# Kernel optimization log

Measured on AMD Instinct MI355X. Metric: run time of the kernel, lower is better.

## Reference

```python
import jax, jax.numpy as jnp
import numpy as np


def setup_inputs() -> dict:
    key = jax.random.key(0)
    ks = jax.random.split(key, 16)
    B, T, A, R, M, D = 128, 1024, 512, 1024, 256, 256  # batch, max_time, annot, rnn, memory, attn dims
    F, K = 32, 31  # location filters, kernel size
    s = jnp.float32(0.02)
    return dict(
        memory=jax.random.normal(ks[0], (B, M), jnp.float32),
        context=jax.random.normal(ks[1], (B, A), jnp.float32),
        rnn_state=jax.random.normal(ks[2], (B, R), jnp.float32),
        annots=jax.random.normal(ks[3], (B, T, A), jnp.float32),
        atten=jax.random.uniform(ks[4], (B, 2, T), jnp.float32),
        mask=jax.random.randint(ks[5], (B, T), 0, 2).astype(jnp.int32),
        Wi=jax.random.normal(ks[6], (3 * R, A + M), jnp.float32) * s,   # GRU input weights (r,z,n)
        Wh=jax.random.normal(ks[7], (3 * R, R), jnp.float32) * s,       # GRU hidden weights
        bi=jnp.zeros((3 * R,), jnp.float32),
        bh=jnp.zeros((3 * R,), jnp.float32),
        conv_w=jax.random.normal(ks[8], (F, 2, K), jnp.float32) * s,    # loc_conv (OIH)
        loc_w=jax.random.normal(ks[9], (D, F), jnp.float32) * s,
        loc_b=jnp.zeros((D,), jnp.float32),
        q_w=jax.random.normal(ks[10], (D, R), jnp.float32) * s,
        q_b=jnp.zeros((D,), jnp.float32),
        a_w=jax.random.normal(ks[11], (D, A), jnp.float32) * s,
        a_b=jnp.zeros((D,), jnp.float32),
        v_w=jax.random.normal(ks[12], (1, D), jnp.float32) * s,
    )


def reference(memory, context, rnn_state, annots, atten, mask,
              Wi, Wh, bi, bh, conv_w, loc_w, loc_b, q_w, q_b, a_w, a_b, v_w):
    # --- GRUCell (torch gate order: r, z, n) ---
    x = jnp.concatenate([memory, context], axis=-1)          # (B, M+A)
    gi = x @ Wi.T + bi                                        # (B, 3R)
    gh = rnn_state @ Wh.T + bh                                # (B, 3R)
    ir, iz, inn = jnp.split(gi, 3, axis=-1)
    hr, hz, hn = jnp.split(gh, 3, axis=-1)
    r = jax.nn.sigmoid(ir + hr)
    z = jax.nn.sigmoid(iz + hz)
    n = jnp.tanh(inn + r * hn)
    h = (1.0 - z) * n + z * rnn_state                         # (B, R) rnn_output

    # --- Location-sensitive attention ---
    pad = (conv_w.shape[-1] - 1) // 2
    loc = jax.lax.conv_general_dilated(atten, conv_w, (1,), [(pad, pad)],
                                       dimension_numbers=('NCH', 'OIH', 'NCH'))  # (B, F, T)
    ploc = jnp.einsum('bft,df->btd', loc, loc_w) + loc_b      # (B, T, D)
    pq = (h @ q_w.T + q_b)[:, None, :]                        # (B, 1, D)
    pa = jnp.einsum('bta,da->btd', annots, a_w) + a_b         # (B, T, D)
    align = jnp.einsum('btd,d->bt', jnp.tanh(pq + pa + ploc), v_w[0])  # (B, T)

    # masked softmax (mask==0 -> -inf)
    align = jnp.where(mask != 0, align, jnp.float32(-1e30))
    align = jax.nn.softmax(align, axis=-1)

    # context = bmm(align, annots)
    ctx = jnp.einsum('bt,bta->ba', align, annots)             # (B, A)
    return (h, ctx, align)
```

## Files before the change

### kernel.cpp

```cpp
#include <hip/hip_runtime.h>
#include <cstddef>

constexpr int B  = 128;
constexpr int T  = 1024;
constexpr int AD = 512;
constexpr int R  = 1024;
constexpr int M  = 256;
constexpr int DD = 256;
constexpr int F  = 32;
constexpr int KW = 31;
constexpr int PADW = 15;
constexpr int XDIM = M + AD;
constexpr int G3 = 3 * R;
constexpr size_t BG3 = (size_t)B * G3;

using short8 = __attribute__((ext_vector_type(8))) short;
using f32x4  = __attribute__((ext_vector_type(4))) float;

__device__ __forceinline__ float sigmoidf(float x) { return 1.f / (1.f + __expf(-x)); }

__device__ __forceinline__ unsigned short f2bf(float x) {
  unsigned int u = __float_as_uint(x);
  u += 0x7FFFu + ((u >> 16) & 1u);
  return (unsigned short)(u >> 16);
}

__device__ __forceinline__ float tanh_fast(float x) {
  float e = __expf(2.f * x);
  return 1.f - 2.f / (e + 1.f);
}

__device__ __forceinline__ uint4 pack_bf8(float4 f0, float4 f1) {
  uint4 r;
  r.x = f2bf(f0.x) | ((unsigned)f2bf(f0.y) << 16);
  r.y = f2bf(f0.z) | ((unsigned)f2bf(f0.w) << 16);
  r.z = f2bf(f1.x) | ((unsigned)f2bf(f1.y) << 16);
  r.w = f2bf(f1.z) | ((unsigned)f2bf(f1.w) << 16);
  return r;
}

__device__ __forceinline__ void load_lds16(const void* g, void* l) {
  __builtin_amdgcn_global_load_lds(
      (const __attribute__((address_space(1))) unsigned int*)g,
      (__attribute__((address_space(3))) unsigned int*)l, 16, 0, 0);
}

__global__ __launch_bounds__(256) void prep_wsw(const float* __restrict__ aw,
                                                const float* __restrict__ lw,
                                                unsigned short* __restrict__ awsw,
                                                unsigned short* __restrict__ lwsw) {
  int idx = blockIdx.x * 256 + threadIdx.x;
  int chunk = idx >> 10;
  int rn = (idx & 1023) >> 2;
  int u = idx & 3;
  int su = u ^ ((rn >> 1) & 3);
  const float* src;
  unsigned short* dst;
  if (chunk < 16) {
    src = aw + (size_t)rn * AD + chunk * 32 + u * 8;
    dst = awsw + chunk * 8192 + rn * 32 + su * 8;
  } else {
    src = lw + (size_t)rn * F + u * 8;
    dst = lwsw + rn * 32 + su * 8;
  }
  float4 f0 = *(const float4*)src;
  float4 f1 = *(const float4*)(src + 4);
  *(uint4*)dst = pack_bf8(f0, f1);
}

__global__ __launch_bounds__(256) void prep_gru(const float* __restrict__ mem,
                                                const float* __restrict__ ctxin,
                                                const float* __restrict__ rnn,
                                                const float* __restrict__ Wi,
                                                const float* __restrict__ Wh,
                                                unsigned short* __restrict__ Wib,
                                                unsigned short* __restrict__ Whb,
                                                unsigned short* __restrict__ xb,
                                                unsigned short* __restrict__ rnnb) {
  const int t = blockIdx.x * 256 + threadIdx.x;
  const float* src;
  unsigned short* dst;
  if (t < 294912) {
    src = Wi + (size_t)t * 8;
    dst = Wib + (size_t)t * 8;
  } else if (t < 688128) {
    size_t e = (size_t)(t - 294912) * 8;
    src = Wh + e;
    dst = Whb + e;
  } else if (t < 700416) {
    size_t e = (size_t)(t - 688128) * 8;
    int row = (int)(e / XDIM), col = (int)(e % XDIM);
    src = (col < M) ? (mem + (size_t)row * M + col)
                    : (ctxin + (size_t)row * AD + (col - M));
    dst = xb + e;
  } else {
    size_t e = (size_t)(t - 700416) * 8;
    src = rnn + e;
    dst = rnnb + e;
  }
  float4 f0 = *(const float4*)src;
  float4 f1 = *(const float4*)(src + 4);
  *(uint4*)dst = pack_bf8(f0, f1);
}

__global__ __launch_bounds__(256) void loc_conv(const float* __restrict__ atten,
                                                const float* __restrict__ conv_w,
                                                unsigned short* __restrict__ locw) {
  __shared__ float s_att[2 * 94];
  __shared__ float s_cw[F * 62];
  const int tid = threadIdx.x;
  const int t0 = blockIdx.x * 64, b = blockIdx.y;
  for (int i = tid; i < 2 * 94; i += 256) {
    int c = i / 94, ii = i - c * 94;
    int gt = t0 - PADW + ii;
    s_att[i] = (gt >= 0 && gt < T) ? atten[((size_t)b * 2 + c) * T + gt] : 0.f;
  }
  for (int i = tid; i < F * 62; i += 256) s_cw[i] = conv_w[i];
  __syncthreads();
  const int f = tid & 31;
  const int tb = (tid >> 5) * 8;
  float a8[8] = {0.f, 0.f, 0.f, 0.f, 0.f, 0.f, 0.f, 0.f};
#pragma unroll
  for (int c = 0; c < 2; ++c) {
    float win[38];
#pragma unroll
    for (int i = 0; i < 38; ++i) win[i] = s_att[c * 94 + tb + i];
#pragma unroll
    for (int k = 0; k < KW; ++k) {
      float w = s_cw[f * 62 + c * 31 + k];
#pragma unroll
      for (int ti = 0; ti < 8; ++ti) a8[ti] += w * win[ti + k];
    }
  }
#pragma unroll
  for (int ti = 0; ti < 8; ++ti)
    locw[((size_t)b * T + t0 + tb + ti) * F + f] = f2bf(a8[ti]);
}

__global__ __launch_bounds__(256, 2) void gemm_gru(const unsigned short* __restrict__ xb,
                                                   const unsigned short* __restrict__ rnnb,
                                                   const unsigned short* __restrict__ Wib,
                                                   const unsigned short* __restrict__ Whb,
                                                   float* __restrict__ outp) {
  const int tid = threadIdx.x;
  const int wv = tid >> 6, lane = tid & 63;
  const int lm = lane & 15, lg = lane >> 4;
  const int g0 = blockIdx.x * 64;
  const int z = blockIdx.y;
  const int which = z >> 2, q = z & 3;
  const unsigned short* __restrict__ A = which ? rnnb : xb;
  const unsigned short* __restrict__ W = which ? Whb : Wib;
  const int K = which ? R : XDIM;
  const int Kq = K >> 2;
  const int nch = Kq >> 5;
  float* __restrict__ C = outp + (size_t)z * BG3;

  const unsigned short* aA = A + (size_t)(wv * 32 + lm) * K + q * Kq + lg * 8;
  const unsigned short* bW = W + (size_t)(g0 + lm) * K + q * Kq + lg * 8;

  f32x4 acc[2][4];
#pragma unroll
  for (int i = 0; i < 2; ++i)
#pragma unroll
    for (int j = 0; j < 4; ++j) acc[i][j] = (f32x4){0.f, 0.f, 0.f, 0.f};

#pragma unroll 2
  for (int ch = 0; ch < nch; ++ch) {
    const int k = ch * 32;
    short8 a8[2], b8[4];
#pragma unroll
    for (int i = 0; i < 2; ++i)
      a8[i] = *(const short8*)(aA + (size_t)i * 16 * K + k);
#pragma unroll
    for (int j = 0; j < 4; ++j)
      b8[j] = *(const short8*)(bW + (size_t)j * 16 * K + k);
#pragma unroll
    for (int j = 0; j < 4; ++j)
#pragma unroll
      for (int i = 0; i < 2; ++i)
        acc[i][j] = __builtin_amdgcn_mfma_f32_16x16x32_bf16(a8[i], b8[j], acc[i][j], 0, 0, 0);
  }

#pragma unroll
  for (int i = 0; i < 2; ++i)
#pragma unroll
    for (int reg = 0; reg < 4; ++reg) {
      const size_t row = (size_t)(wv * 32 + i * 16 + lg * 4 + reg) * G3 + g0 + lm;
#pragma unroll
      for (int j = 0; j < 4; ++j) C[row + j * 16] = acc[i][j][reg];
    }
}

__global__ __launch_bounds__(256) void gru_combine(const float* __restrict__ gp,
                                                   const float* __restrict__ bi,
                                                   const float* __restrict__ bh,
                                                   const float* __restrict__ hprev,
                                                   float* __restrict__ hout) {
  int idx = blockIdx.x * 256 + threadIdx.x;
  int b = idx >> 10, j = idx & (R - 1);
  float ir = bi[j], iz = bi[R + j], inn = bi[2 * R + j];
  float hr = bh[j], hz = bh[R + j], hn = bh[2 * R + j];
#pragma unroll
  for (int z = 0; z < 4; ++z) {
    const float* g = gp + (size_t)z * BG3 + (size_t)b * G3;
    ir += g[j]; iz += g[R + j]; inn += g[2 * R + j];
  }
#pragma unroll
  for (int z = 4; z < 8; ++z) {
    const float* g = gp + (size_t)z * BG3 + (size_t)b * G3;
    hr += g[j]; hz += g[R + j]; hn += g[2 * R + j];
  }
  float r = sigmoidf(ir + hr);
  float z = sigmoidf(iz + hz);
  float n = tanhf(inn + r * hn);
  float hp = hprev[(size_t)b * R + j];
  hout[(size_t)b * R + j] = (1.f - z) * n + z * hp;
}

__global__ __launch_bounds__(256) void pq_kernel(const float* __restrict__ h,
                                                 const float* __restrict__ q_w,
                                                 const float* __restrict__ q_b,
                                                 float* __restrict__ pq) {
  __shared__ __align__(16) float sh[R];
  int b = blockIdx.x, tid = threadIdx.x;
  ((float4*)sh)[tid] = ((const float4*)(h + (size_t)b * R))[tid];
  __syncthreads();
  const float* wr = q_w + (size_t)tid * R;
  float acc = 0.f;
#pragma unroll 4
  for (int k = 0; k < R; k += 4) {
    float4 w = *(const float4*)&wr[k];
    float4 x = *(const float4*)&sh[k];
    acc += w.x * x.x + w.y * x.y + w.z * x.z + w.w * x.w;
  }
  pq[(size_t)b * DD + tid] = acc + q_b[tid];
}

__global__ __launch_bounds__(256, 4) void attn_fused(
    const float* __restrict__ annots, const unsigned short* __restrict__ locw,
    const int* __restrict__ mask,
    const unsigned short* __restrict__ awsw, const unsigned short* __restrict__ lwsw,
    const float* __restrict__ loc_b, const float* __restrict__ a_b,
    const float* __restrict__ v_w, const float* __restrict__ pq,
    float* __restrict__ u_out, float* __restrict__ ctx_part,
    float* __restrict__ S_part) {
  __shared__ __align__(16) unsigned short s_A[2][64 * 32];
  __shared__ __align__(16) unsigned short s_B[2][256 * 32];

  const int tid = threadIdx.x;
  const int wv = tid >> 6, lane = tid & 63;
  const int lm = lane & 15, lg = lane >> 4;
  const int g = blockIdx.x, b = blockIdx.y;
  const int t0 = g * 64;
  const int ar = tid >> 2, au = tid & 3;
  const int asu = au ^ ((ar >> 1) & 3);
  const int sufb = lg ^ ((lm >> 1) & 3);

  const float* arow = annots + ((size_t)b * T + t0 + ar) * AD + au * 8;

  {
    float4 f0 = *(const float4*)(arow);
    float4 f1 = *(const float4*)(arow + 4);
#pragma unroll
    for (int kq = 0; kq < 4; ++kq)
      load_lds16(awsw + wv * 2048 + kq * 512 + lane * 8, &s_B[0][wv * 2048 + kq * 512]);
    *(uint4*)&s_A[0][ar * 32 + asu * 8] = pack_bf8(f0, f1);
  }
  float4 aN0 = *(const float4*)(arow + 32);
  float4 aN1 = *(const float4*)(arow + 36);
  uint4 lvN = {0, 0, 0, 0};

  f32x4 acc[4][4];
#pragma unroll
  for (int j = 0; j < 4; ++j) {
    int d = wv * 64 + j * 16 + lm;
    float base = pq[(size_t)b * DD + d] + a_b[d] + loc_b[d];
    f32x4 bv = {base, base, base, base};
#pragma unroll
    for (int i = 0; i < 4; ++i) acc[i][j] = bv;
  }
  asm volatile("s_waitcnt vmcnt(2) lgkmcnt(0)" ::: "memory");
  __builtin_amdgcn_s_barrier();

#pragma unroll 1
  for (int ks = 0; ks <= 16; ++ks) {
    const int cur = ks & 1, nxt = cur ^ 1;
    if (ks + 1 <= 16) {
      const unsigned short* img = (ks + 1 < 16) ? (awsw + (ks + 1) * 8192) : lwsw;
#pragma unroll
      for (int kq = 0; kq < 4; ++kq)
        load_lds16(img + wv * 2048 + kq * 512 + lane * 8,
                   &s_B[nxt][wv * 2048 + kq * 512]);
    }
    float4 aN20, aN21;
    uint4 lvN2;
    if (ks + 2 <= 15) {
      aN20 = *(const float4*)(arow + (ks + 2) * 32);
      aN21 = *(const float4*)(arow + (ks + 2) * 32 + 4);
    } else if (ks + 2 == 16) {
      lvN2 = *(const uint4*)(locw + ((size_t)b * T + t0 + ar) * F + au * 8);
    }
    if (ks + 1 <= 15) {
      *(uint4*)&s_A[nxt][ar * 32 + asu * 8] = pack_bf8(aN0, aN1);
    } else if (ks + 1 == 16) {
      *(uint4*)&s_A[nxt][ar * 32 + asu * 8] = lvN;
    }
    short8 afr[4], bfr[4];
#pragma unroll
    for (int i = 0; i < 4; ++i)
      afr[i] = *(const short8*)&s_A[cur][(i * 16 + lm) * 32 + sufb * 8];
#pragma unroll
    for (int j = 0; j < 4; ++j)
      bfr[j] = *(const short8*)&s_B[cur][(wv * 64 + j * 16 + lm) * 32 + sufb * 8];
#pragma unroll
    for (int j = 0; j < 4; ++j)
#pragma unroll
      for (int i = 0; i < 4; ++i)
        acc[i][j] = __builtin_amdgcn_mfma_f32_16x16x32_bf16(afr[i], bfr[j], acc[i][j], 0, 0, 0);
    if (ks <= 13) {
      asm volatile("s_waitcnt vmcnt(2) lgkmcnt(0)" ::: "memory");
    } else if (ks == 14) {
      asm volatile("s_waitcnt vmcnt(1) lgkmcnt(0)" ::: "memory");
    } else {
      asm volatile("s_waitcnt vmcnt(0) lgkmcnt(0)" ::: "memory");
    }
    __builtin_amdgcn_s_barrier();
    if (ks + 2 <= 15) { aN0 = aN20; aN1 = aN21; }
    else if (ks + 2 == 16) lvN = lvN2;
  }

  float* s_e = (float*)s_A;
  float* s_u = s_e + 256;
  float vwv[4];
#pragma unroll
  for (int j = 0; j < 4; ++j) vwv[j] = v_w[wv * 64 + j * 16 + lm];
#pragma unroll
  for (int i = 0; i < 4; ++i) {
#pragma unroll
    for (int reg = 0; reg < 4; ++reg) {
      float p = 0.f;
#pragma unroll
      for (int j = 0; j < 4; ++j) p += vwv[j] * tanh_fast(acc[i][j][reg]);
      p += __shfl_xor(p, 1);
      p += __shfl_xor(p, 2);
      p += __shfl_xor(p, 4);
      p += __shfl_xor(p, 8);
      if (lm == 0) s_e[wv * 64 + i * 16 + lg * 4 + reg] = p;
    }
  }
  __syncthreads();
  if (tid < 64) {
    float e = s_e[tid] + s_e[64 + tid] + s_e[128 + tid] + s_e[192 + tid];
    bool mk = mask[(size_t)b * T + t0 + tid] != 0;
    float u = mk ? __expf(e) : 0.f;
    u_out[(size_t)b * T + t0 + tid] = u;
    s_u[tid] = u;
    float p = u;
    p += __shfl_xor(p, 1);
    p += __shfl_xor(p, 2);
    p += __shfl_xor(p, 4);
    p += __shfl_xor(p, 8);
    p += __shfl_xor(p, 16);
    p += __shfl_xor(p, 32);
    if (tid == 0) S_part[b * 16 + g] = p;
  }
  __syncthreads();
  {
    const int a0 = tid * 2;
    const float* ap = annots + ((size_t)b * T + t0) * AD + a0;
    float c0 = 0.f, c1 = 0.f;
#pragma unroll 4
    for (int t = 0; t < 64; ++t) {
      float2 v = *(const float2*)(ap + (size_t)t * AD);
      float w = s_u[t];
      c0 += w * v.x;
      c1 += w * v.y;
    }
    float* dst = ctx_part + (size_t)g * ((size_t)B * AD) + (size_t)b * AD + a0;
    dst[0] = c0;
    dst[1] = c1;
  }
}

__global__ __launch_bounds__(512) void finalize(const float* __restrict__ S_part,
                                                const float* __restrict__ ctx_part,
                                                float* __restrict__ al,
                                                float* __restrict__ ctxo) {
  int b = blockIdx.x, tid = threadIdx.x;
  float S = 0.f;
#pragma unroll
  for (int g = 0; g < 16; ++g) S += S_part[b * 16 + g];
  float inv = 1.f / S;
  float2* ap = (float2*)(al + (size_t)b * T);
  float2 v = ap[tid];
  v.x *= inv; v.y *= inv;
  ap[tid] = v;
  float c = 0.f;
#pragma unroll
  for (int p = 0; p < 16; ++p)
    c += ctx_part[(size_t)p * ((size_t)B * AD) + (size_t)b * AD + tid];
  ctxo[(size_t)b * AD + tid] = c * inv;
}

extern "C" void kernel_launch(void* const* d_in, const int* in_sizes, int n_in,
                              void* d_out, int out_size, void* d_ws, size_t ws_size,
                              hipStream_t stream) {
  const float* memory = (const float*)d_in[0];
  const float* context = (const float*)d_in[1];
  const float* rnn = (const float*)d_in[2];
  const float* annots = (const float*)d_in[3];
  const float* atten = (const float*)d_in[4];
  const int* mask = (const int*)d_in[5];
  const float* Wi = (const float*)d_in[6];
  const float* Wh = (const float*)d_in[7];
  const float* bi = (const float*)d_in[8];
  const float* bh = (const float*)d_in[9];
  const float* conv_w = (const float*)d_in[10];
  const float* loc_w = (const float*)d_in[11];
  const float* loc_b = (const float*)d_in[12];
  const float* q_w = (const float*)d_in[13];
  const float* q_b = (const float*)d_in[14];
  const float* a_w = (const float*)d_in[15];
  const float* a_b = (const float*)d_in[16];
  const float* v_w = (const float*)d_in[17];

  float* out = (float*)d_out;
  float* out_h = out;
  float* out_ctx = out + (size_t)B * R;
  float* out_al = out_ctx + (size_t)B * AD;

  float* ws = (float*)d_ws;
  float* gp_ws = ws;
  float* pq_ws = gp_ws + 8 * BG3;
  float* S_part = pq_ws + (size_t)B * DD;
  float* ctx_part = S_part + (size_t)B * 16;
  unsigned short* awsw = (unsigned short*)(ctx_part + (size_t)16 * B * AD);
  unsigned short* lwsw = awsw + (size_t)16 * 8192;
  unsigned short* locw = lwsw + 8192;
  unsigned short* Wib = locw + (size_t)B * T * F;
  unsigned short* Whb = Wib + (size_t)G3 * XDIM;
  unsigned short* xb = Whb + (size_t)G3 * R;
  unsigned short* rnnb = xb + (size_t)B * XDIM;

  prep_wsw<<<68, 256, 0, stream>>>(a_w, loc_w, awsw, lwsw);
  prep_gru<<<2800, 256, 0, stream>>>(memory, context, rnn, Wi, Wh,
                                     Wib, Whb, xb, rnnb);
  loc_conv<<<dim3(T / 64, B), 256, 0, stream>>>(atten, conv_w, locw);
  gemm_gru<<<dim3(48, 8), 256, 0, stream>>>(xb, rnnb, Wib, Whb, gp_ws);
  gru_combine<<<(B * R) / 256, 256, 0, stream>>>(gp_ws, bi, bh, rnn, out_h);
  pq_kernel<<<B, 256, 0, stream>>>(out_h, q_w, q_b, pq_ws);
  attn_fused<<<dim3(16, B), 256, 0, stream>>>(annots, locw, mask, awsw, lwsw,
                                              loc_b, a_b, v_w, pq_ws,
                                              out_al, ctx_part, S_part);
  finalize<<<B, 512, 0, stream>>>(S_part, ctx_part, out_al, out_ctx);
}
```

Before: 187.5 us.

## Stage whole annots tile in LDS and read weights directly from global

The attention kernel now loads the full 64x512 annots tile (plus location features) into LDS as bf16 up front, instead of double-buffering 32-column slices. The a_w and loc_w B fragments are read straight from global/L2 in plain row-major bf16, dropping the swizzled LDS weight staging. The context reduction then reuses the bf16 annots held in LDS rather than rereading fp32 annots from global memory. The cost is about 70KB of LDS per block, which lowers occupancy (launch bounds 2), gives up load/compute overlap, and makes the context sum use bf16-rounded annots.

```diff
diff --git a/kernel.cpp b/kernel.cpp
--- a/kernel.cpp
+++ b/kernel.cpp
@@ -39,33 +39,17 @@
   return r;
 }
 
-__device__ __forceinline__ void load_lds16(const void* g, void* l) {
-  __builtin_amdgcn_global_load_lds(
-      (const __attribute__((address_space(1))) unsigned int*)g,
-      (__attribute__((address_space(3))) unsigned int*)l, 16, 0, 0);
-}
-
-__global__ __launch_bounds__(256) void prep_wsw(const float* __restrict__ aw,
-                                                const float* __restrict__ lw,
-                                                unsigned short* __restrict__ awsw,
-                                                unsigned short* __restrict__ lwsw) {
+__global__ __launch_bounds__(256) void prep_bf16(const float* __restrict__ aw,
+                                                 const float* __restrict__ lw,
+                                                 unsigned short* __restrict__ awb,
+                                                 unsigned short* __restrict__ lwb) {
   int idx = blockIdx.x * 256 + threadIdx.x;
-  int chunk = idx >> 10;
-  int rn = (idx & 1023) >> 2;
-  int u = idx & 3;
-  int su = u ^ ((rn >> 1) & 3);
-  const float* src;
-  unsigned short* dst;
-  if (chunk < 16) {
-    src = aw + (size_t)rn * AD + chunk * 32 + u * 8;
-    dst = awsw + chunk * 8192 + rn * 32 + su * 8;
+  if (idx < DD * AD) {
+    awb[idx] = f2bf(aw[idx]);
   } else {
-    src = lw + (size_t)rn * F + u * 8;
-    dst = lwsw + rn * 32 + su * 8;
-  }
-  float4 f0 = *(const float4*)src;
-  float4 f1 = *(const float4*)(src + 4);
-  *(uint4*)dst = pack_bf8(f0, f1);
+    int j = idx - DD * AD;
+    if (j < DD * F) lwb[j] = f2bf(lw[j]);
+  }
 }
 
 __global__ __launch_bounds__(256) void prep_gru(const float* __restrict__ mem,
@@ -236,16 +220,16 @@
   pq[(size_t)b * DD + tid] = acc + q_b[tid];
 }
 
-__global__ __launch_bounds__(256, 4) void attn_fused(
+__global__ __launch_bounds__(256, 2) void attn_fused(
     const float* __restrict__ annots, const unsigned short* __restrict__ locw,
     const int* __restrict__ mask,
-    const unsigned short* __restrict__ awsw, const unsigned short* __restrict__ lwsw,
+    const unsigned short* __restrict__ awb, const unsigned short* __restrict__ lwb,
     const float* __restrict__ loc_b, const float* __restrict__ a_b,
     const float* __restrict__ v_w, const float* __restrict__ pq,
     float* __restrict__ u_out, float* __restrict__ ctx_part,
     float* __restrict__ S_part) {
-  __shared__ __align__(16) unsigned short s_A[2][64 * 32];
-  __shared__ __align__(16) unsigned short s_B[2][256 * 32];
+  __shared__ __align__(16) unsigned short s_A[17 * 2048];
+  __shared__ float s_sc[256 + 64];
 
   const int tid = threadIdx.x;
   const int wv = tid >> 6, lane = tid & 63;
@@ -257,18 +241,16 @@
   const int sufb = lg ^ ((lm >> 1) & 3);
 
   const float* arow = annots + ((size_t)b * T + t0 + ar) * AD + au * 8;
-
+#pragma unroll 4
+  for (int ks = 0; ks < 16; ++ks) {
+    float4 f0 = *(const float4*)(arow + ks * 32);
+    float4 f1 = *(const float4*)(arow + ks * 32 + 4);
+    *(uint4*)&s_A[ks * 2048 + ar * 32 + asu * 8] = pack_bf8(f0, f1);
+  }
   {
-    float4 f0 = *(const float4*)(arow);
-    float4 f1 = *(const float4*)(arow + 4);
-#pragma unroll
-    for (int kq = 0; kq < 4; ++kq)
-      load_lds16(awsw + wv * 2048 + kq * 512 + lane * 8, &s_B[0][wv * 2048 + kq * 512]);
-    *(uint4*)&s_A[0][ar * 32 + asu * 8] = pack_bf8(f0, f1);
-  }
-  float4 aN0 = *(const float4*)(arow + 32);
-  float4 aN1 = *(const float4*)(arow + 36);
-  uint4 lvN = {0, 0, 0, 0};
+    uint4 lv = *(const uint4*)(locw + ((size_t)b * T + t0 + ar) * F + au * 8);
+    *(uint4*)&s_A[16 * 2048 + ar * 32 + asu * 8] = lv;
+  }
 
   f32x4 acc[4][4];
 #pragma unroll
@@ -279,58 +261,42 @@
 #pragma unroll
     for (int i = 0; i < 4; ++i) acc[i][j] = bv;
   }
-  asm volatile("s_waitcnt vmcnt(2) lgkmcnt(0)" ::: "memory");
-  __builtin_amdgcn_s_barrier();
-
-#pragma unroll 1
-  for (int ks = 0; ks <= 16; ++ks) {
-    const int cur = ks & 1, nxt = cur ^ 1;
-    if (ks + 1 <= 16) {
-      const unsigned short* img = (ks + 1 < 16) ? (awsw + (ks + 1) * 8192) : lwsw;
-#pragma unroll
-      for (int kq = 0; kq < 4; ++kq)
-        load_lds16(img + wv * 2048 + kq * 512 + lane * 8,
-                   &s_B[nxt][wv * 2048 + kq * 512]);
-    }
-    float4 aN20, aN21;
-    uint4 lvN2;
-    if (ks + 2 <= 15) {
-      aN20 = *(const float4*)(arow + (ks + 2) * 32);
-      aN21 = *(const float4*)(arow + (ks + 2) * 32 + 4);
-    } else if (ks + 2 == 16) {
-      lvN2 = *(const uint4*)(locw + ((size_t)b * T + t0 + ar) * F + au * 8);
-    }
-    if (ks + 1 <= 15) {
-      *(uint4*)&s_A[nxt][ar * 32 + asu * 8] = pack_bf8(aN0, aN1);
-    } else if (ks + 1 == 16) {
-      *(uint4*)&s_A[nxt][ar * 32 + asu * 8] = lvN;
-    }
+  __syncthreads();
+
+  const unsigned short* bW = awb + (size_t)(wv * 64 + lm) * AD + lg * 8;
+#pragma unroll 2
+  for (int ks = 0; ks < 16; ++ks) {
     short8 afr[4], bfr[4];
 #pragma unroll
     for (int i = 0; i < 4; ++i)
-      afr[i] = *(const short8*)&s_A[cur][(i * 16 + lm) * 32 + sufb * 8];
-#pragma unroll
-    for (int j = 0; j < 4; ++j)
-      bfr[j] = *(const short8*)&s_B[cur][(wv * 64 + j * 16 + lm) * 32 + sufb * 8];
+      afr[i] = *(const short8*)&s_A[ks * 2048 + (i * 16 + lm) * 32 + sufb * 8];
+#pragma unroll
+    for (int j = 0; j < 4; ++j)
+      bfr[j] = *(const short8*)(bW + (size_t)j * 16 * AD + ks * 32);
 #pragma unroll
     for (int j = 0; j < 4; ++j)
 #pragma unroll
       for (int i = 0; i < 4; ++i)
         acc[i][j] = __builtin_amdgcn_mfma_f32_16x16x32_bf16(afr[i], bfr[j], acc[i][j], 0, 0, 0);
-    if (ks <= 13) {
-      asm volatile("s_waitcnt vmcnt(2) lgkmcnt(0)" ::: "memory");
-    } else if (ks == 14) {
-      asm volatile("s_waitcnt vmcnt(1) lgkmcnt(0)" ::: "memory");
-    } else {
-      asm volatile("s_waitcnt vmcnt(0) lgkmcnt(0)" ::: "memory");
-    }
-    __builtin_amdgcn_s_barrier();
-    if (ks + 2 <= 15) { aN0 = aN20; aN1 = aN21; }
-    else if (ks + 2 == 16) lvN = lvN2;
-  }
-
-  float* s_e = (float*)s_A;
-  float* s_u = s_e + 256;
+  }
+  {
+    const unsigned short* bWl = lwb + (size_t)(wv * 64 + lm) * F + lg * 8;
+    short8 afr[4], bfr[4];
+#pragma unroll
+    for (int i = 0; i < 4; ++i)
+      afr[i] = *(const short8*)&s_A[16 * 2048 + (i * 16 + lm) * 32 + sufb * 8];
+#pragma unroll
+    for (int j = 0; j < 4; ++j)
+      bfr[j] = *(const short8*)(bWl + (size_t)j * 16 * F);
+#pragma unroll
+    for (int j = 0; j < 4; ++j)
+#pragma unroll
+      for (int i = 0; i < 4; ++i)
+        acc[i][j] = __builtin_amdgcn_mfma_f32_16x16x32_bf16(afr[i], bfr[j], acc[i][j], 0, 0, 0);
+  }
+
+  float* s_e = s_sc;
+  float* s_u = s_sc + 256;
   float vwv[4];
 #pragma unroll
   for (int j = 0; j < 4; ++j) vwv[j] = v_w[wv * 64 + j * 16 + lm];
@@ -367,14 +333,16 @@
   __syncthreads();
   {
     const int a0 = tid * 2;
-    const float* ap = annots + ((size_t)b * T + t0) * AD + a0;
+    const int c = a0 >> 5, uu = (a0 & 31) >> 3, ee = a0 & 7;
+    const unsigned short* base = s_A + c * 2048;
     float c0 = 0.f, c1 = 0.f;
 #pragma unroll 4
     for (int t = 0; t < 64; ++t) {
-      float2 v = *(const float2*)(ap + (size_t)t * AD);
+      int su = uu ^ ((t >> 1) & 3);
+      unsigned int v = *(const unsigned int*)&base[t * 32 + su * 8 + ee];
       float w = s_u[t];
-      c0 += w * v.x;
-      c1 += w * v.y;
+      c0 += w * __uint_as_float((v & 0xFFFFu) << 16);
+      c1 += w * __uint_as_float(v & 0xFFFF0000u);
     }
     float* dst = ctx_part + (size_t)g * ((size_t)B * AD) + (size_t)b * AD + a0;
     dst[0] = c0;
@@ -434,22 +402,22 @@
   float* pq_ws = gp_ws + 8 * BG3;
   float* S_part = pq_ws + (size_t)B * DD;
   float* ctx_part = S_part + (size_t)B * 16;
-  unsigned short* awsw = (unsigned short*)(ctx_part + (size_t)16 * B * AD);
-  unsigned short* lwsw = awsw + (size_t)16 * 8192;
-  unsigned short* locw = lwsw + 8192;
+  unsigned short* awb = (unsigned short*)(ctx_part + (size_t)16 * B * AD);
+  unsigned short* lwb = awb + (size_t)DD * AD;
+  unsigned short* locw = lwb + (size_t)DD * F;
   unsigned short* Wib = locw + (size_t)B * T * F;
   unsigned short* Whb = Wib + (size_t)G3 * XDIM;
   unsigned short* xb = Whb + (size_t)G3 * R;
   unsigned short* rnnb = xb + (size_t)B * XDIM;
 
-  prep_wsw<<<68, 256, 0, stream>>>(a_w, loc_w, awsw, lwsw);
+  prep_bf16<<<(DD * AD + DD * F) / 256, 256, 0, stream>>>(a_w, loc_w, awb, lwb);
   prep_gru<<<2800, 256, 0, stream>>>(memory, context, rnn, Wi, Wh,
                                      Wib, Whb, xb, rnnb);
   loc_conv<<<dim3(T / 64, B), 256, 0, stream>>>(atten, conv_w, locw);
   gemm_gru<<<dim3(48, 8), 256, 0, stream>>>(xb, rnnb, Wib, Whb, gp_ws);
   gru_combine<<<(B * R) / 256, 256, 0, stream>>>(gp_ws, bi, bh, rnn, out_h);
   pq_kernel<<<B, 256, 0, stream>>>(out_h, q_w, q_b, pq_ws);
-  attn_fused<<<dim3(16, B), 256, 0, stream>>>(annots, locw, mask, awsw, lwsw,
+  attn_fused<<<dim3(16, B), 256, 0, stream>>>(annots, locw, mask, awb, lwb,
                                               loc_b, a_b, v_w, pq_ws,
                                               out_al, ctx_part, S_part);
   finalize<<<B, 512, 0, stream>>>(S_part, ctx_part, out_al, out_ctx);
```

Measured after the change: 206.7 us. +10.3%, slower.
